# Performance work log

Measured on AMD Instinct MI355X. Metric: run time of the kernel, lower is better.

The kernel has to match this reference:

```python
import jax, jax.numpy as jnp
import numpy as np

B, L, D, NHEAD, NLAYERS = 2, 2048, 256, 8, 8
NAMES = ['self', 'cross'] * 4


def setup_inputs() -> dict:
    key = jax.random.key(0)
    ks = jax.random.split(key, 6)
    w_scale = D ** -0.5  # keep activations well-scaled
    return {
        'f0': jax.random.normal(ks[0], (B, L, D), dtype=jnp.float32),
        'f1': jax.random.normal(ks[1], (B, L, D), dtype=jnp.float32),
        'Wq': jax.random.normal(ks[2], (NLAYERS, D, D), dtype=jnp.float32) * w_scale,
        'Wk': jax.random.normal(ks[3], (NLAYERS, D, D), dtype=jnp.float32) * w_scale,
        'Wv': jax.random.normal(ks[4], (NLAYERS, D, D), dtype=jnp.float32) * w_scale,
        'Wo': jax.random.normal(ks[5], (NLAYERS, D, D), dtype=jnp.float32) * w_scale,
    }


def _rope(x, inv_freq):
    # x: (B, L, D); RoPE over the FULL model dim (matches original, mixes heads)
    L_, D_ = x.shape[1], x.shape[2]
    t = jnp.arange(L_, dtype=jnp.float32)
    freqs = t[:, None] * inv_freq[None, :]          # (L, D/2)
    emb = jnp.concatenate([freqs, freqs], axis=-1)  # (L, D)
    x1, x2 = x[..., : D_ // 2], x[..., D_ // 2:]
    rot = jnp.concatenate([-x2, x1], axis=-1)
    return x * jnp.cos(emb) + rot * jnp.sin(emb)


def _attn(x, src, wq, wk, wv, wo, use_rope, inv_freq):
    b, l1, d = x.shape
    l2 = src.shape[1]
    dh = d // NHEAD
    q = x @ wq.T    # torch Linear: x @ W^T
    k = src @ wk.T
    v = src @ wv.T
    if use_rope:
        q = _rope(q, inv_freq)
        k = _rope(k, inv_freq)
    q = q.reshape(b, l1, NHEAD, dh)
    k = k.reshape(b, l2, NHEAD, dh)
    v = v.reshape(b, l2, NHEAD, dh)
    scores = jnp.einsum('bqhd,bkhd->bhqk', q, k) * (dh ** -0.5)
    out = jnp.einsum('bhqk,bkhd->bqhd', jax.nn.softmax(scores, axis=-1), v)
    return out.reshape(b, l1, d) @ wo.T


def reference(f0, f1, Wq, Wk, Wv, Wo):
    d = f0.shape[-1]
    inv_freq = 1.0 / (10000.0 ** (jnp.arange(0, d, 2, dtype=jnp.float32) / d))
    for i, name in enumerate(NAMES):
        if name == 'self':
            f0 = f0 + _attn(f0, f0, Wq[i], Wk[i], Wv[i], Wo[i], True, inv_freq)
            f1 = f1 + _attn(f1, f1, Wq[i], Wk[i], Wv[i], Wo[i], True, inv_freq)
        else:
            # sequential updates: second cross uses the UPDATED f0 (matches torch)
            f0 = f0 + _attn(f0, f1, Wq[i], Wk[i], Wv[i], Wo[i], False, inv_freq)
            f1 = f1 + _attn(f1, f0, Wq[i], Wk[i], Wv[i], Wo[i], False, inv_freq)
    return (f0, f1)
```

## Files before the change

### kernel.cpp

```cpp
#include <hip/hip_runtime.h>

#define BB   2
#define LL   2048
#define DD   256
#define NH   8
#define MM   (BB*LL)
#define NLAYERS 8
#define MMDD ((size_t)MM*DD)

typedef unsigned short ushort_t;
typedef __attribute__((ext_vector_type(8))) short  short8;
typedef __attribute__((ext_vector_type(4))) float  f32x4;
typedef __attribute__((ext_vector_type(4))) unsigned int u32x4;
typedef __attribute__((ext_vector_type(2))) unsigned int u32x2;

#define CSC 0.2550500394f

#define WAITV2 asm volatile("s_waitcnt vmcnt(2)" ::: "memory")
#define WAITV4 asm volatile("s_waitcnt vmcnt(4)" ::: "memory")
#define WAITV0 asm volatile("s_waitcnt vmcnt(0)" ::: "memory")
#define BAR()  __builtin_amdgcn_s_barrier()
#define SCHED0 __builtin_amdgcn_sched_barrier(0)

__device__ __forceinline__ f32x4 mfma16(short8 a, short8 b, f32x4 c) {
    return __builtin_amdgcn_mfma_f32_16x16x32_bf16(a, b, c, 0, 0, 0);
}
__device__ __forceinline__ unsigned cvtpk(float lo, float hi) {
    unsigned r;
    asm volatile("v_cvt_pk_bf16_f32 %0, %1, %2" : "=v"(r) : "v"(lo), "v"(hi));
    return r;
}
__device__ __forceinline__ void pl32(unsigned &a, unsigned &b) {
    asm volatile("v_permlane32_swap_b32 %0, %1" : "+v"(a), "+v"(b));
}
__device__ __forceinline__ float bf2f(unsigned short h) {
    return __builtin_bit_cast(float, ((unsigned)h) << 16);
}
__device__ __forceinline__ void gll16(const void* gsrc, void* ldst) {
    __builtin_amdgcn_global_load_lds(
        (const __attribute__((address_space(1))) unsigned int*)gsrc,
        (__attribute__((address_space(3))) unsigned int*)ldst, 16, 0, 0);
}


__global__ __launch_bounds__(256) void convbf(const float* __restrict__ in,
                                              ushort_t* __restrict__ out, int n8) {
    int i = blockIdx.x * 256 + threadIdx.x;
    if (i >= n8) return;
    const f32x4* p = (const f32x4*)(in + (size_t)i * 8);
    f32x4 a = p[0], b = p[1];
    u32x4 o = {cvtpk(a.x, a.y), cvtpk(a.z, a.w), cvtpk(b.x, b.y), cvtpk(b.z, b.w)};
    *(u32x4*)&out[(size_t)i * 8] = o;
}

__global__ __launch_bounds__(256) void wconv(const float* __restrict__ a,
                                             const float* __restrict__ b,
                                             const float* __restrict__ c,
                                             const float* __restrict__ d,
                                             ushort_t* __restrict__ out) {
    int i = blockIdx.x * 256 + threadIdx.x;
    int reg = i >> 16, loc = i & 65535;
    const float* src = reg == 0 ? a : reg == 1 ? b : reg == 2 ? c : d;
    const f32x4* p = (const f32x4*)(src + (size_t)loc * 8);
    f32x4 x = p[0], y = p[1];
    u32x4 o = {cvtpk(x.x, x.y), cvtpk(x.z, x.w), cvtpk(y.x, y.y), cvtpk(y.z, y.w)};
    *(u32x4*)&out[(size_t)reg * 524288 + (size_t)loc * 8] = o;
}

__global__ __launch_bounds__(128) void rtab(float* __restrict__ tab) {
    int p = blockIdx.x, j = threadIdx.x;
    float inv = __expf(-((float)j / 128.f) * 9.210340371976184f);
    float s, c;
    sincosf((float)p * inv, &s, &c);
    tab[(size_t)p * 256 + j]       = c;
    tab[(size_t)p * 256 + 128 + j] = s;
}

__global__ __launch_bounds__(256) void rope_qk(ushort_t* __restrict__ Qio,
                                               const ushort_t* __restrict__ KSrc,
                                               ushort_t* __restrict__ KT,
                                               const float* __restrict__ tab) {
    const bool isq = (blockIdx.y == 0);
    const ushort_t* S = isq ? Qio : KSrc;
    int t = threadIdx.x;
    int row = blockIdx.x * 8 + (t >> 5);
    int jj = (t & 31) * 4;
    int pos = row & (LL - 1);
    u32x2 va = *(const u32x2*)&S[(size_t)row * 256 + jj];
    u32x2 vb = *(const u32x2*)&S[(size_t)row * 256 + 128 + jj];
    f32x4 a = {bf2f(va.x & 0xffff), bf2f(va.x >> 16),
               bf2f(va.y & 0xffff), bf2f(va.y >> 16)};
    f32x4 b = {bf2f(vb.x & 0xffff), bf2f(vb.x >> 16),
               bf2f(vb.y & 0xffff), bf2f(vb.y >> 16)};
    f32x4 c = *(const f32x4*)&tab[(size_t)pos * 256 + jj];
    f32x4 s = *(const f32x4*)&tab[(size_t)pos * 256 + 128 + jj];
    f32x4 o1 = a * c - b * s;
    f32x4 o2 = b * c + a * s;
    if (isq) { o1 *= CSC; o2 *= CSC; }
    u32x2 p1 = {cvtpk(o1.x, o1.y), cvtpk(o1.z, o1.w)};
    u32x2 p2 = {cvtpk(o2.x, o2.y), cvtpk(o2.z, o2.w)};
    if (isq) {
        *(u32x2*)&Qio[(size_t)row * 256 + jj]       = p1;
        *(u32x2*)&Qio[(size_t)row * 256 + 128 + jj] = p2;
    } else {
        int z = row >> 11, key = row & 2047;
        int tt = key >> 6, kk = key & 63;
        int hA = jj >> 5, dh = jj & 31;
        int g = dh >> 3, e = dh & 7;
        size_t base = (size_t)tt * 2048 + (size_t)g * 512 + (size_t)kk * 8 + e;
        *(u32x2*)&KT[(size_t)(z * 8 + hA) * 65536 + base]     = p1;
        *(u32x2*)&KT[(size_t)(z * 8 + hA + 4) * 65536 + base] = p2;
    }
}

template<int NQ, int NK, int NV, int QMODE, int KMODE, int NTY>
__global__ __launch_bounds__(256) void gemm5(const ushort_t* __restrict__ X,
                                             const ushort_t* __restrict__ WQ,
                                             const ushort_t* __restrict__ WK,
                                             const ushort_t* __restrict__ WV,
                                             ushort_t* __restrict__ DQ,
                                             ushort_t* __restrict__ DK,
                                             ushort_t* __restrict__ DVT,
                                             const float* __restrict__ Res,
                                             float* __restrict__ OutF) {
    constexpr int NTX = NQ + NK + NV;
    __shared__ ushort_t Xb[3][4096];
    __shared__ ushort_t Wb[3][4096];
    const int tid = threadIdx.x, ln = tid & 63, w = tid >> 6;
    const int f = blockIdx.x;
    const int xcd = f & 7, s = f >> 3;
    const int bx = s % NTX, byg = s / NTX;
    const int by = xcd * (NTY / 8) + byg;
    const int m0 = by * 64;

    const ushort_t* W; ushort_t* DH; int n0, mode;
    if (NQ && bx < NQ)           { W = WQ; DH = DQ;  mode = QMODE; n0 = bx * 64; }
    else if (NK && bx < NQ + NK) { W = WK; DH = DK;  mode = KMODE; n0 = (bx - NQ) * 64; }
    else                         { W = WV; DH = DVT; mode = 3; n0 = (bx - NQ - NK) * 64; }

    auto stage = [&](int c, int buf) {
#pragma unroll
        for (int i = 0; i < 2; i++) {
            int sl = (w * 2 + i) * 64 + ln;
            int r = sl >> 3, x = sl & 7;
            int col = c * 64 + ((x ^ (r & 7)) << 3);
            gll16(X + (size_t)(m0 + r) * 256 + col, &Xb[buf][(w * 2 + i) * 512]);
            gll16(W + (size_t)(n0 + r) * 256 + col, &Wb[buf][(w * 2 + i) * 512]);
        }
    };

    const int ql = ln & 15, gq = ln >> 4;
    const int wm = w >> 1, wn = w & 1;
    f32x4 z4 = {0.f, 0.f, 0.f, 0.f};
    f32x4 acc[2][2] = {{z4, z4}, {z4, z4}};

    stage(0, 0);
    stage(1, 1);
#pragma unroll
    for (int c = 0; c < 4; c++) {
        if (c < 3) { WAITV4; } else { WAITV0; }
        BAR(); SCHED0;
        if (c + 2 < 4) stage(c + 2, (c + 2) % 3);
        const ushort_t* XL = Xb[c % 3];
        const ushort_t* WL = Wb[c % 3];
        __builtin_amdgcn_s_setprio(1);
#pragma unroll
        for (int ks = 0; ks < 2; ks++) {
            int cc = ks * 4 + gq;
            int r0 = 32 * wm + ql, r1 = r0 + 16;
            int nr0 = 32 * wn + ql, nr1 = nr0 + 16;
            short8 a0 = *(const short8*)&XL[(r0 * 8 + (cc ^ (r0 & 7))) * 8];
            short8 a1 = *(const short8*)&XL[(r1 * 8 + (cc ^ (r1 & 7))) * 8];
            short8 b0 = *(const short8*)&WL[(nr0 * 8 + (cc ^ (nr0 & 7))) * 8];
            short8 b1 = *(const short8*)&WL[(nr1 * 8 + (cc ^ (nr1 & 7))) * 8];
            acc[0][0] = mfma16(a0, b0, acc[0][0]);
            acc[0][1] = mfma16(a0, b1, acc[0][1]);
            acc[1][0] = mfma16(a1, b0, acc[1][0]);
            acc[1][1] = mfma16(a1, b1, acc[1][1]);
        }
        __builtin_amdgcn_s_setprio(0);
    }

    if (mode == 3) {
        float* scr = (float*)&Xb[0][0];
        __syncthreads();
#pragma unroll
        for (int mf = 0; mf < 2; mf++)
#pragma unroll
            for (int nf = 0; nf < 2; nf++)
#pragma unroll
                for (int r = 0; r < 4; r++) {
                    int nloc = 32 * wn + 16 * nf + ql;
                    int mloc = 32 * wm + 16 * mf + 4 * gq + r;
                    scr[nloc * 65 + mloc] = acc[mf][nf][r];
                }
        __syncthreads();
        int nloc = tid >> 2, mc = (tid & 3) * 16;
        int ng = n0 + nloc, hh = ng >> 5, dh = ng & 31;
        int mg = m0 + mc;
        int z = mg >> 11, key = mg & 2047;
        int tt = key >> 6;
        int ks = (mc >> 5) & 1, J = (mc >> 4) & 1;
        int cA = 4 * ks + 2 * J, cB = cA + 1;
        int swz = dh & 7;
        const float* sc = &scr[nloc * 65 + mc];
        u32x2 q0 = {cvtpk(sc[0], sc[1]),   cvtpk(sc[2], sc[3])};
        u32x2 q1 = {cvtpk(sc[4], sc[5]),   cvtpk(sc[6], sc[7])};
        u32x2 q2 = {cvtpk(sc[8], sc[9]),   cvtpk(sc[10], sc[11])};
        u32x2 q3 = {cvtpk(sc[12], sc[13]), cvtpk(sc[14], sc[15])};
        ushort_t* base = &DVT[(size_t)(z * 8 + hh) * 65536 + (size_t)tt * 2048 + dh * 64];
        *(u32x2*)&base[(cA ^ swz) * 8]     = q0;
        *(u32x2*)&base[(cB ^ swz) * 8]     = q1;
        *(u32x2*)&base[(cA ^ swz) * 8 + 4] = q2;
        *(u32x2*)&base[(cB ^ swz) * 8 + 4] = q3;
    } else {
#pragma unroll
        for (int mf = 0; mf < 2; mf++)
#pragma unroll
            for (int nf = 0; nf < 2; nf++)
#pragma unroll
                for (int r = 0; r < 4; r++) {
                    int mg = m0 + 32 * wm + 16 * mf + gq * 4 + r;
                    int ng = n0 + 32 * wn + 16 * nf + ql;
                    float v = acc[mf][nf][r];
                    if (mode == 1) {
                        size_t idx = (size_t)mg * 256 + ng;
                        float o = Res[idx] + v;
                        OutF[idx] = o;
                        DH[idx] = (ushort_t)cvtpk(o, o);
                    } else if (mode == 2) {
                        DH[(size_t)mg * 256 + ng] = (ushort_t)cvtpk(v, v);
                    } else if (mode == 5) {
                        int zh = (mg >> 11) * 8 + (ng >> 5);
                        size_t off = (size_t)zh * 65536
                                   + (size_t)((mg & 2047) >> 6) * 2048
                                   + (size_t)((ng & 31) >> 3) * 512
                                   + (size_t)(mg & 63) * 8 + (ng & 7);
                        DH[off] = (ushort_t)cvtpk(v, v);
                    } else {
                        float vs = v * CSC;
                        DH[(size_t)mg * 256 + ng] = (ushort_t)cvtpk(vs, vs);
                    }
                }
    }
}

template<int SPLIT>
__global__ __launch_bounds__(256) void attn8(const ushort_t* __restrict__ Q,
                                             const ushort_t* __restrict__ K,
                                             const ushort_t* __restrict__ Vt,
                                             float* __restrict__ Op,
                                             float* __restrict__ Lp, int mrows) {
    constexpr int KEYS = 2048 / SPLIT;
    constexpr int NT = KEYS / 64;
    __shared__ ushort_t K_lds[3][2048];
    __shared__ ushort_t V_lds[3][2048];

    const int tid = threadIdx.x, ln = tid & 63, w = tid >> 6;
    const int ql = ln & 15, gq = ln >> 4;
    const int f = blockIdx.x;
    const int xcd = f & 7, slot = f >> 3;
    const int qb = slot & 15, gg = slot >> 4;
    const int h = xcd;
    const int zz = gg / SPLIT, sp = gg % SPLIT;
    const int q0 = qb * 128 + w * 32;
    const size_t rb = (size_t)zz * 2048;
    const int zh = zz * 8 + h;

    short8 qfA = *(const short8*)&Q[(rb + q0 + ql) * 256 + h * 32 + gq * 8];
    short8 qfB = *(const short8*)&Q[(rb + q0 + 16 + ql) * 256 + h * 32 + gq * 8];

    const ushort_t* kt = K  + (size_t)zh * 65536 + (size_t)sp * NT * 2048 + tid * 8;
    const ushort_t* vt = Vt + (size_t)zh * 65536 + (size_t)sp * NT * 2048 + tid * 8;

    gll16(kt,        &K_lds[0][w * 512]);
    gll16(vt,        &V_lds[0][w * 512]);
    gll16(kt + 2048, &K_lds[1][w * 512]);
    gll16(vt + 2048, &V_lds[1][w * 512]);

    const short os = (short)0x3F80;
    const short8 ones = {os, os, os, os, os, os, os, os};
    f32x4 z4 = {0.f, 0.f, 0.f, 0.f};
    f32x4 o0A = z4, o1A = z4, o0B = z4, o1B = z4, laccA = z4, laccB = z4;

    int cur = 0, pre = 2;
    for (int t = 0; t < NT; t++) {
        if (t < NT - 1) { WAITV2; } else { WAITV0; }
        BAR(); SCHED0;
        if (t + 2 < NT) {
            gll16(kt + (size_t)(t + 2) * 2048, &K_lds[pre][w * 512]);
            gll16(vt + (size_t)(t + 2) * 2048, &V_lds[pre][w * 512]);
        }
        const ushort_t* KL = K_lds[cur];
        const ushort_t* VL = V_lds[cur];

        f32x4 stA[4], stB[4];
        __builtin_amdgcn_s_setprio(1);
#pragma unroll
        for (int j = 0; j < 4; j++) {
            short8 kf = *(const short8*)&KL[(gq * 64 + 16 * j + ql) * 8];
            stA[j] = mfma16(kf, qfA, z4);
            stB[j] = mfma16(kf, qfB, z4);
        }
        __builtin_amdgcn_s_setprio(0);
#pragma unroll
        for (int j = 0; j < 4; j++)
#pragma unroll
            for (int r = 0; r < 4; r++) {
                stA[j][r] = __builtin_amdgcn_exp2f(stA[j][r]);
                stB[j][r] = __builtin_amdgcn_exp2f(stB[j][r]);
            }
        unsigned aLo[4], aHi[4], bLo[4], bHi[4];
#pragma unroll
        for (int j = 0; j < 4; j++) {
            aLo[j] = cvtpk(stA[j][0], stA[j][1]);
            aHi[j] = cvtpk(stA[j][2], stA[j][3]);
            bLo[j] = cvtpk(stB[j][0], stB[j][1]);
            bHi[j] = cvtpk(stB[j][2], stB[j][3]);
        }
        pl32(aLo[0], aLo[1]); pl32(aHi[0], aHi[1]);
        pl32(aLo[2], aLo[3]); pl32(aHi[2], aHi[3]);
        pl32(bLo[0], bLo[1]); pl32(bHi[0], bHi[1]);
        pl32(bLo[2], bLo[3]); pl32(bHi[2], bHi[3]);
        u32x4 fA0 = {aLo[0], aHi[0], aLo[1], aHi[1]};
        u32x4 fA1 = {aLo[2], aHi[2], aLo[3], aHi[3]};
        u32x4 fB0 = {bLo[0], bHi[0], bLo[1], bHi[1]};
        u32x4 fB1 = {bLo[2], bHi[2], bLo[3], bHi[3]};
        short8 pfA[2] = {__builtin_bit_cast(short8, fA0),
                         __builtin_bit_cast(short8, fA1)};
        short8 pfB[2] = {__builtin_bit_cast(short8, fB0),
                         __builtin_bit_cast(short8, fB1)};

        __builtin_amdgcn_s_setprio(1);
#pragma unroll
        for (int ks = 0; ks < 2; ks++) {
            int sw = (4 * ks + gq) ^ (ql & 7);
            short8 vf0 = *(const short8*)&VL[(ql * 8 + sw) * 8];
            short8 vf1 = *(const short8*)&VL[((16 + ql) * 8 + sw) * 8];
            o0A = mfma16(vf0, pfA[ks], o0A);
            o1A = mfma16(vf1, pfA[ks], o1A);
            o0B = mfma16(vf0, pfB[ks], o0B);
            o1B = mfma16(vf1, pfB[ks], o1B);
            laccA = mfma16(ones, pfA[ks], laccA);
            laccB = mfma16(ones, pfB[ks], laccB);
        }
        __builtin_amdgcn_s_setprio(0);
        cur = (cur == 2) ? 0 : cur + 1;
        pre = (pre == 2) ? 0 : pre + 1;
    }

    size_t rowA = rb + q0 + ql, rowB = rowA + 16;
    float* obA = Op + (size_t)sp * mrows * 256 + rowA * 256 + h * 32;
    float* obB = Op + (size_t)sp * mrows * 256 + rowB * 256 + h * 32;
    *(f32x4*)&obA[gq * 4]      = o0A;
    *(f32x4*)&obA[16 + gq * 4] = o1A;
    *(f32x4*)&obB[gq * 4]      = o0B;
    *(f32x4*)&obB[16 + gq * 4] = o1B;
    if (gq == 0) {
        Lp[(size_t)sp * mrows * 8 + rowA * 8 + h] = laccA[0];
        Lp[(size_t)sp * mrows * 8 + rowB * 8 + h] = laccB[0];
    }
}

template<int SPLIT>
__global__ __launch_bounds__(256) void combine(const float* __restrict__ Op,
                                               const float* __restrict__ Lp,
                                               ushort_t* __restrict__ Out,
                                               int mrows) {
    int t = threadIdx.x;
    size_t r = (size_t)blockIdx.x * 8 + (t >> 5);
    int c0 = (t & 31) * 8, h = c0 >> 5;
    float l = 0.f;
    f32x4 a = {0.f, 0.f, 0.f, 0.f}, b = a;
#pragma unroll
    for (int sp = 0; sp < SPLIT; sp++) {
        l += Lp[(size_t)sp * mrows * 8 + r * 8 + h];
        a += *(const f32x4*)&Op[(size_t)sp * mrows * 256 + r * 256 + c0];
        b += *(const f32x4*)&Op[(size_t)sp * mrows * 256 + r * 256 + c0 + 4];
    }
    float inv = 1.f / l;
    u32x4 o = {cvtpk(a.x * inv, a.y * inv), cvtpk(a.z * inv, a.w * inv),
               cvtpk(b.x * inv, b.y * inv), cvtpk(b.z * inv, b.w * inv)};
    *(u32x4*)&Out[r * 256 + c0] = o;
}

extern "C" void kernel_launch(void* const* d_in, const int* in_sizes, int n_in,
                              void* d_out, int out_size, void* d_ws, size_t ws_size,
                              hipStream_t stream) {
    const float* f0_in = (const float*)d_in[0];
    const float* f1_in = (const float*)d_in[1];
    const float* Wq = (const float*)d_in[2];
    const float* Wk = (const float*)d_in[3];
    const float* Wv = (const float*)d_in[4];
    const float* Wo = (const float*)d_in[5];

    float* F0 = (float*)d_out;
    float* F1 = F0 + MMDD;

    ushort_t* Fb  = (ushort_t*)d_ws;
    ushort_t* Qb  = Fb  + 2 * MMDD;
    ushort_t* Khb = Qb  + 2 * MMDD;
    ushort_t* Vhb = Khb + 2 * MMDD;
    ushort_t* Tbb = Vhb + 2 * MMDD;
    ushort_t* Wb  = Tbb + 2 * MMDD;
    float*    Opw = (float*)(Wb + 2 * MMDD);
    float*    Lpw = Opw + (size_t)4 * MMDD;
    float*    tab = Lpw + 262144;

    ushort_t* Wqb = Wb;
    ushort_t* Wkb = Wb + (size_t)NLAYERS * 65536;
    ushort_t* Wvb = Wb + (size_t)2 * NLAYERS * 65536;
    ushort_t* Wob = Wb + (size_t)3 * NLAYERS * 65536;

    const size_t fbytes = MMDD * sizeof(float);
    hipMemcpyAsync(F0, f0_in, fbytes, hipMemcpyDeviceToDevice, stream);
    hipMemcpyAsync(F1, f1_in, fbytes, hipMemcpyDeviceToDevice, stream);
    convbf<<<1024, 256, 0, stream>>>(F0, Fb, 262144);
    wconv<<<1024, 256, 0, stream>>>(Wq, Wk, Wv, Wo, Wb);
    rtab<<<LL, 128, 0, stream>>>(tab);

    for (int i = 0; i < NLAYERS; i++) {
        const ushort_t* wq = Wqb + (size_t)i * 65536;
        const ushort_t* wk = Wkb + (size_t)i * 65536;
        const ushort_t* wv = Wvb + (size_t)i * 65536;
        const ushort_t* wo = Wob + (size_t)i * 65536;

        if ((i & 1) == 0) {
            gemm5<4, 4, 4, 2, 2, 128><<<1536, 256, 0, stream>>>(
                Fb, wq, wk, wv, Qb, Tbb, Vhb, nullptr, nullptr);
            rope_qk<<<dim3(1024, 2), 256, 0, stream>>>(Qb, Tbb, Khb, tab);
            attn8<2><<<1024, 256, 0, stream>>>(Qb, Khb, Vhb, Opw, Lpw, MM * 2);
            combine<2><<<1024, 256, 0, stream>>>(Opw, Lpw, Tbb, MM * 2);
            gemm5<4, 0, 0, 1, 0, 128><<<512, 256, 0, stream>>>(
                Tbb, wo, nullptr, nullptr, Fb, nullptr, nullptr, F0, F0);
        } else {
            gemm5<4, 0, 0, 4, 0, 128><<<512, 256, 0, stream>>>(
                Fb, wq, nullptr, nullptr, Qb, nullptr, nullptr, nullptr, nullptr);
            for (int s = 0; s < 2; s++) {
                const ushort_t* sb = Fb + (size_t)(1 - s) * MMDD;
                float* xf = s ? F1 : F0;
                ushort_t* xbw = Fb + (size_t)s * MMDD;
                gemm5<0, 4, 4, 0, 5, 64><<<512, 256, 0, stream>>>(
                    sb, nullptr, wk, wv, nullptr, Khb, Vhb, nullptr, nullptr);
                attn8<4><<<1024, 256, 0, stream>>>(Qb + (size_t)s * MMDD,
                                                   Khb, Vhb, Opw, Lpw, MM);
                combine<4><<<512, 256, 0, stream>>>(Opw, Lpw, Tbb, MM);
                gemm5<4, 0, 0, 1, 0, 64><<<256, 256, 0, stream>>>(
                    Tbb, wo, nullptr, nullptr, xbw, nullptr, nullptr, xf, xf);
            }
        }
    }
}
```

Measured before the change: 571.9 us.

## Fuse split-attention combine into output projection GEMM and merge init copies

Removes the separate combine kernel by having a new output-projection GEMM reduce the split-K attention partials (O and L), normalise them and write the bf16 tile straight into shared memory before the MFMA loop. The launch sequence also replaces the two device-to-device memcpys plus bf16 conversion with one init kernel that copies and converts both inputs. This saves a bf16 intermediate write and read plus several launches per layer. In exchange, each output block re-reads the fp32 partials for its 64 rows across all four column tiles, so the partial reads are duplicated, and the kernel uses a larger shared-memory footprint.

```diff
diff --git a/kernel.cpp b/kernel.cpp
--- a/kernel.cpp
+++ b/kernel.cpp
@@ -17,8 +17,8 @@
 #define CSC 0.2550500394f
 
 #define WAITV2 asm volatile("s_waitcnt vmcnt(2)" ::: "memory")
-#define WAITV4 asm volatile("s_waitcnt vmcnt(4)" ::: "memory")
 #define WAITV0 asm volatile("s_waitcnt vmcnt(0)" ::: "memory")
+#define WAITLG asm volatile("s_waitcnt lgkmcnt(0)" ::: "memory")
 #define BAR()  __builtin_amdgcn_s_barrier()
 #define SCHED0 __builtin_amdgcn_sched_barrier(0)
 
@@ -43,14 +43,19 @@
 }
 
 
-__global__ __launch_bounds__(256) void convbf(const float* __restrict__ in,
-                                              ushort_t* __restrict__ out, int n8) {
+__global__ __launch_bounds__(256) void initf(const float* __restrict__ f0,
+                                             const float* __restrict__ f1,
+                                             float* __restrict__ F,
+                                             ushort_t* __restrict__ Fb) {
     int i = blockIdx.x * 256 + threadIdx.x;
-    if (i >= n8) return;
-    const f32x4* p = (const f32x4*)(in + (size_t)i * 8);
+    const float* src = (i < 131072) ? f0 : f1;
+    int loc = i & 131071;
+    const f32x4* p = (const f32x4*)(src + (size_t)loc * 8);
     f32x4 a = p[0], b = p[1];
+    *(f32x4*)&F[(size_t)i * 8]     = a;
+    *(f32x4*)&F[(size_t)i * 8 + 4] = b;
     u32x4 o = {cvtpk(a.x, a.y), cvtpk(a.z, a.w), cvtpk(b.x, b.y), cvtpk(b.z, b.w)};
-    *(u32x4*)&out[(size_t)i * 8] = o;
+    *(u32x4*)&Fb[(size_t)i * 8] = o;
 }
 
 __global__ __launch_bounds__(256) void wconv(const float* __restrict__ a,
@@ -120,9 +125,7 @@
                                              const ushort_t* __restrict__ WV,
                                              ushort_t* __restrict__ DQ,
                                              ushort_t* __restrict__ DK,
-                                             ushort_t* __restrict__ DVT,
-                                             const float* __restrict__ Res,
-                                             float* __restrict__ OutF) {
+                                             ushort_t* __restrict__ DVT) {
     constexpr int NTX = NQ + NK + NV;
     __shared__ ushort_t Xb[3][4096];
     __shared__ ushort_t Wb[3][4096];
@@ -158,7 +161,7 @@
     stage(1, 1);
 #pragma unroll
     for (int c = 0; c < 4; c++) {
-        if (c < 3) { WAITV4; } else { WAITV0; }
+        if (c < 3) { asm volatile("s_waitcnt vmcnt(4)" ::: "memory"); } else { WAITV0; }
         BAR(); SCHED0;
         if (c + 2 < 4) stage(c + 2, (c + 2) % 3);
         const ushort_t* XL = Xb[c % 3];
@@ -223,12 +226,7 @@
                     int mg = m0 + 32 * wm + 16 * mf + gq * 4 + r;
                     int ng = n0 + 32 * wn + 16 * nf + ql;
                     float v = acc[mf][nf][r];
-                    if (mode == 1) {
-                        size_t idx = (size_t)mg * 256 + ng;
-                        float o = Res[idx] + v;
-                        OutF[idx] = o;
-                        DH[idx] = (ushort_t)cvtpk(o, o);
-                    } else if (mode == 2) {
+                    if (mode == 2) {
                         DH[(size_t)mg * 256 + ng] = (ushort_t)cvtpk(v, v);
                     } else if (mode == 5) {
                         int zh = (mg >> 11) * 8 + (ng >> 5);
@@ -245,6 +243,113 @@
     }
 }
 
+template<int SPLIT, int NTY>
+__global__ __launch_bounds__(256) void gemmO(const float* __restrict__ Op,
+                                             const float* __restrict__ Lp,
+                                             const ushort_t* __restrict__ W,
+                                             const float* __restrict__ Res,
+                                             float* __restrict__ OutF,
+                                             ushort_t* __restrict__ OutH,
+                                             int mrows) {
+    __shared__ ushort_t Xf[64 * 256];
+    __shared__ ushort_t Wpb[3][4096];
+    const int tid = threadIdx.x, ln = tid & 63, w = tid >> 6;
+    const int f = blockIdx.x;
+    const int xcd = f & 7, s = f >> 3;
+    const int bx = s & 3, byg = s >> 2;
+    const int by = xcd * (NTY / 8) + byg;
+    const int m0 = by * 64, n0 = bx * 64;
+
+    auto stageW = [&](int c, int buf) {
+#pragma unroll
+        for (int i = 0; i < 2; i++) {
+            int sl = (w * 2 + i) * 64 + ln;
+            int r = sl >> 3, x = sl & 7;
+            int col = c * 64 + ((x ^ (r & 7)) << 3);
+            gll16(W + (size_t)(n0 + r) * 256 + col, &Wpb[buf][(w * 2 + i) * 512]);
+        }
+    };
+    stageW(0, 0);
+    stageW(1, 1);
+
+    const int xr = tid >> 2, q = tid & 3, hb = q >> 1;
+    float inv[4];
+#pragma unroll
+    for (int hh = 0; hh < 4; hh++) {
+        float l = 0.f;
+#pragma unroll
+        for (int sp = 0; sp < SPLIT; sp++)
+            l += Lp[(size_t)sp * mrows * 8 + (size_t)(m0 + xr) * 8 + 2 * hh + hb];
+        inv[hh] = 1.f / l;
+    }
+#pragma unroll
+    for (int p = 0; p < 4; p++) {
+        int col = q * 16 + 64 * p;
+        f32x4 a0 = {0.f,0.f,0.f,0.f}, a1 = a0, a2 = a0, a3 = a0;
+#pragma unroll
+        for (int sp = 0; sp < SPLIT; sp++) {
+            const float* src = &Op[(size_t)sp * mrows * 256 + (size_t)(m0 + xr) * 256 + col];
+            a0 += *(const f32x4*)&src[0];
+            a1 += *(const f32x4*)&src[4];
+            a2 += *(const f32x4*)&src[8];
+            a3 += *(const f32x4*)&src[12];
+        }
+        float iv = inv[p];
+        a0 *= iv; a1 *= iv; a2 *= iv; a3 *= iv;
+        u32x4 w0 = {cvtpk(a0.x, a0.y), cvtpk(a0.z, a0.w),
+                    cvtpk(a1.x, a1.y), cvtpk(a1.z, a1.w)};
+        u32x4 w1 = {cvtpk(a2.x, a2.y), cvtpk(a2.z, a2.w),
+                    cvtpk(a3.x, a3.y), cvtpk(a3.z, a3.w)};
+        int xc0 = q * 2;
+        *(u32x4*)&Xf[xr * 256 + p * 64 + ((xc0)     ^ (xr & 7)) * 8] = w0;
+        *(u32x4*)&Xf[xr * 256 + p * 64 + ((xc0 + 1) ^ (xr & 7)) * 8] = w1;
+    }
+    WAITLG;
+    BAR(); SCHED0;
+
+    const int ql = ln & 15, gq = ln >> 4;
+    const int wm = w >> 1, wn = w & 1;
+    f32x4 z4 = {0.f, 0.f, 0.f, 0.f};
+    f32x4 acc[2][2] = {{z4, z4}, {z4, z4}};
+#pragma unroll
+    for (int c = 0; c < 4; c++) {
+        if (c < 3) { WAITV2; } else { WAITV0; }
+        BAR(); SCHED0;
+        if (c + 2 < 4) stageW(c + 2, (c + 2) % 3);
+        const ushort_t* WL = Wpb[c % 3];
+        __builtin_amdgcn_s_setprio(1);
+#pragma unroll
+        for (int ks = 0; ks < 2; ks++) {
+            int cc = ks * 4 + gq;
+            int r0 = 32 * wm + ql, r1 = r0 + 16;
+            int nr0 = 32 * wn + ql, nr1 = nr0 + 16;
+            short8 a0 = *(const short8*)&Xf[r0 * 256 + c * 64 + (cc ^ (r0 & 7)) * 8];
+            short8 a1 = *(const short8*)&Xf[r1 * 256 + c * 64 + (cc ^ (r1 & 7)) * 8];
+            short8 b0 = *(const short8*)&WL[(nr0 * 8 + (cc ^ (nr0 & 7))) * 8];
+            short8 b1 = *(const short8*)&WL[(nr1 * 8 + (cc ^ (nr1 & 7))) * 8];
+            acc[0][0] = mfma16(a0, b0, acc[0][0]);
+            acc[0][1] = mfma16(a0, b1, acc[0][1]);
+            acc[1][0] = mfma16(a1, b0, acc[1][0]);
+            acc[1][1] = mfma16(a1, b1, acc[1][1]);
+        }
+        __builtin_amdgcn_s_setprio(0);
+    }
+
+#pragma unroll
+    for (int mf = 0; mf < 2; mf++)
+#pragma unroll
+        for (int nf = 0; nf < 2; nf++)
+#pragma unroll
+            for (int r = 0; r < 4; r++) {
+                int mg = m0 + 32 * wm + 16 * mf + gq * 4 + r;
+                int ng = n0 + 32 * wn + 16 * nf + ql;
+                size_t idx = (size_t)mg * 256 + ng;
+                float o = Res[idx] + acc[mf][nf][r];
+                OutF[idx] = o;
+                OutH[idx] = (ushort_t)cvtpk(o, o);
+            }
+}
+
 template<int SPLIT>
 __global__ __launch_bounds__(256) void attn8(const ushort_t* __restrict__ Q,
                                              const ushort_t* __restrict__ K,
@@ -326,10 +431,10 @@
         u32x4 fA1 = {aLo[2], aHi[2], aLo[3], aHi[3]};
         u32x4 fB0 = {bLo[0], bHi[0], bLo[1], bHi[1]};
         u32x4 fB1 = {bLo[2], bHi[2], bLo[3], bHi[3]};
-        short8 pfA[2] = {__builtin_bit_cast(short8, fA0),
-                         __builtin_bit_cast(short8, fA1)};
-        short8 pfB[2] = {__builtin_bit_cast(short8, fB0),
-                         __builtin_bit_cast(short8, fB1)};
+        short8 pfA0 = __builtin_bit_cast(short8, fA0);
+        short8 pfA1 = __builtin_bit_cast(short8, fA1);
+        short8 pfB0 = __builtin_bit_cast(short8, fB0);
+        short8 pfB1 = __builtin_bit_cast(short8, fB1);
 
         __builtin_amdgcn_s_setprio(1);
 #pragma unroll
@@ -337,12 +442,14 @@
             int sw = (4 * ks + gq) ^ (ql & 7);
             short8 vf0 = *(const short8*)&VL[(ql * 8 + sw) * 8];
             short8 vf1 = *(const short8*)&VL[((16 + ql) * 8 + sw) * 8];
-            o0A = mfma16(vf0, pfA[ks], o0A);
-            o1A = mfma16(vf1, pfA[ks], o1A);
-            o0B = mfma16(vf0, pfB[ks], o0B);
-            o1B = mfma16(vf1, pfB[ks], o1B);
-            laccA = mfma16(ones, pfA[ks], laccA);
-            laccB = mfma16(ones, pfB[ks], laccB);
+            short8 pA = ks ? pfA1 : pfA0;
+            short8 pB = ks ? pfB1 : pfB0;
+            o0A = mfma16(vf0, pA, o0A);
+            o1A = mfma16(vf1, pA, o1A);
+            o0B = mfma16(vf0, pB, o0B);
+            o1B = mfma16(vf1, pB, o1B);
+            laccA = mfma16(ones, pA, laccA);
+            laccB = mfma16(ones, pB, laccB);
         }
         __builtin_amdgcn_s_setprio(0);
         cur = (cur == 2) ? 0 : cur + 1;
@@ -362,28 +469,6 @@
     }
 }
 
-template<int SPLIT>
-__global__ __launch_bounds__(256) void combine(const float* __restrict__ Op,
-                                               const float* __restrict__ Lp,
-                                               ushort_t* __restrict__ Out,
-                                               int mrows) {
-    int t = threadIdx.x;
-    size_t r = (size_t)blockIdx.x * 8 + (t >> 5);
-    int c0 = (t & 31) * 8, h = c0 >> 5;
-    float l = 0.f;
-    f32x4 a = {0.f, 0.f, 0.f, 0.f}, b = a;
-#pragma unroll
-    for (int sp = 0; sp < SPLIT; sp++) {
-        l += Lp[(size_t)sp * mrows * 8 + r * 8 + h];
-        a += *(const f32x4*)&Op[(size_t)sp * mrows * 256 + r * 256 + c0];
-        b += *(const f32x4*)&Op[(size_t)sp * mrows * 256 + r * 256 + c0 + 4];
-    }
-    float inv = 1.f / l;
-    u32x4 o = {cvtpk(a.x * inv, a.y * inv), cvtpk(a.z * inv, a.w * inv),
-               cvtpk(b.x * inv, b.y * inv), cvtpk(b.z * inv, b.w * inv)};
-    *(u32x4*)&Out[r * 256 + c0] = o;
-}
-
 extern "C" void kernel_launch(void* const* d_in, const int* in_sizes, int n_in,
                               void* d_out, int out_size, void* d_ws, size_t ws_size,
                               hipStream_t stream) {
@@ -412,10 +497,7 @@
     ushort_t* Wvb = Wb + (size_t)2 * NLAYERS * 65536;
     ushort_t* Wob = Wb + (size_t)3 * NLAYERS * 65536;
 
-    const size_t fbytes = MMDD * sizeof(float);
-    hipMemcpyAsync(F0, f0_in, fbytes, hipMemcpyDeviceToDevice, stream);
-    hipMemcpyAsync(F1, f1_in, fbytes, hipMemcpyDeviceToDevice, stream);
-    convbf<<<1024, 256, 0, stream>>>(F0, Fb, 262144);
+    initf<<<1024, 256, 0, stream>>>(f0_in, f1_in, F0, Fb);
     wconv<<<1024, 256, 0, stream>>>(Wq, Wk, Wv, Wo, Wb);
     rtab<<<LL, 128, 0, stream>>>(tab);
 
@@ -427,26 +509,22 @@
 
         if ((i & 1) == 0) {
             gemm5<4, 4, 4, 2, 2, 128><<<1536, 256, 0, stream>>>(
-                Fb, wq, wk, wv, Qb, Tbb, Vhb, nullptr, nullptr);
+                Fb, wq, wk, wv, Qb, Tbb, Vhb);
             rope_qk<<<dim3(1024, 2), 256, 0, stream>>>(Qb, Tbb, Khb, tab);
             attn8<2><<<1024, 256, 0, stream>>>(Qb, Khb, Vhb, Opw, Lpw, MM * 2);
-            combine<2><<<1024, 256, 0, stream>>>(Opw, Lpw, Tbb, MM * 2);
-            gemm5<4, 0, 0, 1, 0, 128><<<512, 256, 0, stream>>>(
-                Tbb, wo, nullptr, nullptr, Fb, nullptr, nullptr, F0, F0);
+            gemmO<2, 128><<<512, 256, 0, stream>>>(Opw, Lpw, wo, F0, F0, Fb, MM * 2);
         } else {
             gemm5<4, 0, 0, 4, 0, 128><<<512, 256, 0, stream>>>(
-                Fb, wq, nullptr, nullptr, Qb, nullptr, nullptr, nullptr, nullptr);
+                Fb, wq, nullptr, nullptr, Qb, nullptr, nullptr);
             for (int s = 0; s < 2; s++) {
                 const ushort_t* sb = Fb + (size_t)(1 - s) * MMDD;
                 float* xf = s ? F1 : F0;
                 ushort_t* xbw = Fb + (size_t)s * MMDD;
                 gemm5<0, 4, 4, 0, 5, 64><<<512, 256, 0, stream>>>(
-                    sb, nullptr, wk, wv, nullptr, Khb, Vhb, nullptr, nullptr);
+                    sb, nullptr, wk, wv, nullptr, Khb, Vhb);
                 attn8<4><<<1024, 256, 0, stream>>>(Qb + (size_t)s * MMDD,
                                                    Khb, Vhb, Opw, Lpw, MM);
-                combine<4><<<512, 256, 0, stream>>>(Opw, Lpw, Tbb, MM);
-                gemm5<4, 0, 0, 1, 0, 64><<<256, 256, 0, stream>>>(
-                    Tbb, wo, nullptr, nullptr, xbw, nullptr, nullptr, xf, xf);
+                gemmO<4, 64><<<256, 256, 0, stream>>>(Opw, Lpw, wo, xf, xf, xbw, MM);
             }
         }
     }
```

Result: no change. 570.0 us (-0.3%).
